# Performance work log

Measured on AMD Instinct MI355X. Metric: run time of the kernel, lower is better.

Reference implementation:

```python
import jax, jax.numpy as jnp
import numpy as np

N, K = 16384, 16          # nodes, neighbors per node
IN, HID, OUT = 256, 512, 512
HEADS, A = 8, 64          # heads * attention_size = 512
EPS = 1e-5


def _layernorm(x, g, b):
    m = x.mean(-1, keepdims=True)
    v = x.var(-1, keepdims=True)
    return (x - m) / jnp.sqrt(v + EPS) * g + b


def setup_inputs() -> dict:
    key = jax.random.key(0)
    ks = jax.random.split(key, 16)
    def lin(k, i, o):
        kw, kb = jax.random.split(k)
        w = jax.random.normal(kw, (i, o), jnp.float32) / np.sqrt(i).astype(np.float32)
        b = jax.random.normal(kb, (o,), jnp.float32) * 0.01
        return w, b
    inp = {}
    inp["data"] = jax.random.normal(ks[0], (N, IN), jnp.float32)
    inp["neighbors"] = jax.random.randint(ks[1], (N, K), 0, N, jnp.int32)
    inp["mlp_w0"], inp["mlp_b0"] = lin(ks[2], IN, HID)
    inp["mlp_w1"], inp["mlp_b1"] = lin(ks[3], HID, HID)
    inp["mlp_w2"], inp["mlp_b2"] = lin(ks[4], HID, HID)
    inp["pd_w"], inp["pd_b"] = lin(ks[5], IN, HID)   # project_down
    inp["pi_w"], inp["pi_b"] = lin(ks[6], IN, OUT)   # project_in
    inp["q_w"], inp["q_b"] = lin(ks[7], HID, HEADS * A)
    inp["k_w"], inp["k_b"] = lin(ks[8], HID, HEADS * A)
    inp["v_w"], inp["v_b"] = lin(ks[9], HID, HEADS * A)
    inp["o_w"], inp["o_b"] = lin(ks[10], HEADS * A, OUT)
    inp["ln1_g"] = jnp.ones((HID,), jnp.float32)
    inp["ln1_b"] = jnp.zeros((HID,), jnp.float32)
    inp["ln2_g"] = jnp.ones((OUT,), jnp.float32)
    inp["ln2_b"] = jnp.zeros((OUT,), jnp.float32)
    return inp


def reference(data, neighbors, mlp_w0, mlp_b0, mlp_w1, mlp_b1, mlp_w2, mlp_b2,
              pd_w, pd_b, pi_w, pi_b, q_w, q_b, k_w, k_b, v_w, v_b, o_w, o_b,
              ln1_g, ln1_b, ln2_g, ln2_b):
    # --- local MLP branch (3-layer MLP, elu between layers) ---
    h = jax.nn.elu(data @ mlp_w0 + mlp_b0)
    h = jax.nn.elu(h @ mlp_w1 + mlp_b1)
    h = h @ mlp_w2 + mlp_b2
    pd = data @ pd_w + pd_b                 # project_down(data), reused twice
    local = h + pd                          # MLP(data) + project_down(data)
    # dropout is identity in eval mode
    local = jax.nn.elu(_layernorm(local + pd, ln1_g, ln1_b))
    # --- neighbour dot multi-head attention ---
    q = (local @ q_w + q_b).reshape(N, HEADS, A)
    kk = (local @ k_w + k_b)
    vv = (local @ v_w + v_b)
    kn = kk[neighbors].reshape(N, K, HEADS, A)   # irregular gather
    vn = vv[neighbors].reshape(N, K, HEADS, A)
    scores = jnp.einsum('nha,nkha->nhk', q, kn) / np.float32(np.sqrt(A))
    w = jax.nn.softmax(scores, axis=-1)
    attn = jnp.einsum('nhk,nkha->nha', w, vn).reshape(N, HEADS * A)
    interaction = attn @ o_w + o_b
    # --- residual + output norm ---
    return _layernorm(interaction + data @ pi_w + pi_b, ln2_g, ln2_b)
```

## Files before the change

### kernel.cpp

```cpp
#include <hip/hip_runtime.h>

typedef _Float16 h16;
typedef _Float16 h16x8 __attribute__((ext_vector_type(8)));
typedef _Float16 h16x4 __attribute__((ext_vector_type(4)));
typedef _Float16 h16x2 __attribute__((ext_vector_type(2)));
typedef float f32x4 __attribute__((ext_vector_type(4)));

#define DEV static __device__ __forceinline__

static constexpr size_t OFF_DATA = 0;
static constexpr size_t OFF_W0T  = 4194304;
static constexpr size_t OFF_W1T  = 4325376;
static constexpr size_t OFF_W2PD = 4587520;
static constexpr size_t OFF_QKVT = 4980736;
static constexpr size_t OFF_OPIT = 5767168;
static constexpr size_t OFF_X1   = 6160384;
static constexpr size_t OFF_X2   = 14548992;
static constexpr size_t OFF_KV   = OFF_X1;
static constexpr size_t OFF_P    = 22937600;

DEV void gload16(const void* g, void* l)
{
    __builtin_amdgcn_global_load_lds(
        (__attribute__((address_space(1))) void*)(void*)g,
        (__attribute__((address_space(3))) void*)l, 16, 0, 0);
}

DEV float eluf(float x) { return x > 0.f ? x : __expf(x) - 1.f; }

__global__ __launch_bounds__(256)
void k_cvt_data(const float* __restrict__ src, h16* __restrict__ dst)
{
    size_t i = ((size_t)blockIdx.x * 256 + threadIdx.x) * 4;
    float4 v = *(const float4*)(src + i);
    h16x4 o;
    o[0] = (h16)v.x; o[1] = (h16)v.y; o[2] = (h16)v.z; o[3] = (h16)v.w;
    *(h16x4*)(dst + i) = o;
}

__global__ void k_prep_w(const float* __restrict__ w0, const float* __restrict__ w1,
                         const float* __restrict__ w2, const float* __restrict__ pdw,
                         const float* __restrict__ qw, const float* __restrict__ kw,
                         const float* __restrict__ vw, const float* __restrict__ ow,
                         const float* __restrict__ piw, h16* __restrict__ ws)
{
    int b = blockIdx.x;
    const float* src; h16* dst; int K, dstStride, dstKOff = 0, tb; float scale = 1.f;
    const int N = 512;
    if (b < 128)       { src = w0;  dst = ws + OFF_W0T;           K = 256; dstStride = 256; tb = 0; }
    else if (b < 384)  { src = w1;  dst = ws + OFF_W1T;           K = 512; dstStride = 512; tb = 128; }
    else if (b < 640)  { src = w2;  dst = ws + OFF_W2PD;          K = 512; dstStride = 768; tb = 384; }
    else if (b < 768)  { src = pdw; dst = ws + OFF_W2PD;          K = 256; dstStride = 768; dstKOff = 512; scale = 2.f; tb = 640; }
    else if (b < 1024) { src = qw;  dst = ws + OFF_QKVT;          K = 512; dstStride = 512; tb = 768; }
    else if (b < 1280) { src = kw;  dst = ws + OFF_QKVT + 262144; K = 512; dstStride = 512; tb = 1024; }
    else if (b < 1536) { src = vw;  dst = ws + OFF_QKVT + 524288; K = 512; dstStride = 512; tb = 1280; }
    else if (b < 1792) { src = ow;  dst = ws + OFF_OPIT;          K = 512; dstStride = 768; tb = 1536; }
    else               { src = piw; dst = ws + OFF_OPIT;          K = 256; dstStride = 768; dstKOff = 512; tb = 1792; }
    int t = b - tb;
    int tilesK = K >> 5;
    int tk = t % tilesK, tn = t / tilesK;
    __shared__ float tile[32][33];
    int tx = threadIdx.x, ty = threadIdx.y;
    #pragma unroll
    for (int r = 0; r < 32; r += 8)
        tile[ty + r][tx] = src[(size_t)(tk * 32 + ty + r) * N + tn * 32 + tx] * scale;
    __syncthreads();
    #pragma unroll
    for (int r = 0; r < 32; r += 8) {
        int n = tn * 32 + ty + r, k = tk * 32 + tx;
        dst[(size_t)n * dstStride + dstKOff + k] = (h16)tile[tx][ty + r];
    }
}

template<int BIASMODE, bool DOELU>
__global__ __launch_bounds__(512, 4)
void k_gemm(const h16* __restrict__ A1, const h16* __restrict__ A2,
            const int K1, const int K2,
            const h16* __restrict__ BT,
            const float* __restrict__ bias1, const float* __restrict__ bias2,
            const float* __restrict__ bias3, const float b2scale,
            h16* __restrict__ out, h16* __restrict__ out2, const int N)
{
    const int Kt = K1 + K2;
    __shared__ __align__(16) h16 sA[128 * 32];
    __shared__ __align__(16) h16 sB[128 * 32];
    const int tid  = threadIdx.x;
    const int lane = tid & 63;
    const int mBase = blockIdx.y * 128, nBase = blockIdx.x * 128;
    const int w  = tid >> 6;
    const int wm = (w >> 2) * 64;
    const int wn = (w & 3) * 32;
    const f32x4 zero = {0.f, 0.f, 0.f, 0.f};
    f32x4 acc[4][2];
    #pragma unroll
    for (int i = 0; i < 4; ++i) {
        #pragma unroll
        for (int j = 0; j < 2; ++j) acc[i][j] = zero;
    }

    const int ldR = tid >> 2;
    const int ldC = (tid & 3) * 8;
    const int lm = lane & 15, lk = (lane >> 4) * 8;

    for (int k0 = 0; k0 < Kt; k0 += 32) {
        const h16* Ab; int Ak, As;
        if (k0 < K1) { Ab = A1; Ak = k0;      As = K1; }
        else         { Ab = A2; Ak = k0 - K1; As = K2; }
        gload16(Ab + (size_t)(mBase + ldR) * As + Ak + ldC, &sA[ldR * 32 + ldC]);
        gload16(BT + (size_t)(nBase + ldR) * Kt + k0 + ldC, &sB[ldR * 32 + ldC]);
        __syncthreads();
        h16x8 af[4], bfr[2];
        #pragma unroll
        for (int i = 0; i < 4; ++i) af[i]  = *(const h16x8*)&sA[(wm + i * 16 + lm) * 32 + lk];
        #pragma unroll
        for (int j = 0; j < 2; ++j) bfr[j] = *(const h16x8*)&sB[(wn + j * 16 + lm) * 32 + lk];
        #pragma unroll
        for (int i = 0; i < 4; ++i) {
            #pragma unroll
            for (int j = 0; j < 2; ++j)
                acc[i][j] = __builtin_amdgcn_mfma_f32_16x16x32_f16(af[i], bfr[j], acc[i][j], 0, 0, 0);
        }
        __syncthreads();
    }

    const int lr4 = (lane >> 4) * 4;
    #pragma unroll
    for (int j = 0; j < 2; ++j) {
        const int col = nBase + wn + j * 16 + lm;
        float bv;
        if (BIASMODE == 0) bv = bias1[col];
        else if (BIASMODE == 1) bv = bias1[col] + b2scale * bias2[col];
        else {
            const int seg = col >> 9;
            const float* bp = seg == 0 ? bias1 : (seg == 1 ? bias2 : bias3);
            bv = bp[col & 511];
        }
        #pragma unroll
        for (int i = 0; i < 4; ++i) {
            const int row0 = mBase + wm + i * 16 + lr4;
            #pragma unroll
            for (int r = 0; r < 4; ++r) {
                float v = acc[i][j][r] + bv;
                if (DOELU) v = eluf(v);
                if (BIASMODE == 2) {
                    if (col < 512) out [(size_t)(row0 + r) * 512  + col]         = (h16)v;
                    else           out2[(size_t)(row0 + r) * 1024 + (col - 512)] = (h16)v;
                } else {
                    out[(size_t)(row0 + r) * N + col] = (h16)v;
                }
            }
        }
    }
}

template<bool DOELU, bool OUTF32>
__global__ __launch_bounds__(256)
void k_ln(const h16* __restrict__ X, const float* __restrict__ g, const float* __restrict__ b,
          h16* __restrict__ outH, float* __restrict__ outF)
{
    const int row  = blockIdx.x * 4 + (threadIdx.x >> 6);
    const int lane = threadIdx.x & 63;
    const h16x8 xv = *(const h16x8*)(X + (size_t)row * 512 + lane * 8);
    float v[8], s = 0.f, ss = 0.f;
    #pragma unroll
    for (int k = 0; k < 8; ++k) { v[k] = (float)xv[k]; s += v[k]; ss += v[k] * v[k]; }
    #pragma unroll
    for (int m = 1; m < 64; m <<= 1) { s += __shfl_xor(s, m, 64); ss += __shfl_xor(ss, m, 64); }
    const float mean = s * (1.f / 512.f);
    const float var  = ss * (1.f / 512.f) - mean * mean;
    const float rstd = rsqrtf(var + 1e-5f);
    #pragma unroll
    for (int k = 0; k < 8; ++k) {
        const int c = lane * 8 + k;
        float y = (v[k] - mean) * rstd * g[c] + b[c];
        if (DOELU) y = eluf(y);
        if (OUTF32) outF[(size_t)row * 512 + c] = y;
        else        outH[(size_t)row * 512 + c] = (h16)y;
    }
}

__global__ __launch_bounds__(256)
void k_attn(const h16* __restrict__ Q, const h16* __restrict__ KV,
            const int* __restrict__ nbr, h16* __restrict__ outA)
{
    const int n = blockIdx.x;
    const int tid = threadIdx.x, lane = tid & 63, wave = tid >> 6;
    __shared__ float sS[8][16];
    __shared__ float sW[8][16];
    __shared__ __align__(16) float sP[2][512];
    const int h = lane >> 3;
    const int cbase = lane * 8;
    const int isV = wave >> 1;
    const int jbase = (wave & 1) * 8;

    h16x8 rows[8];
    #pragma unroll
    for (int r = 0; r < 8; ++r) {
        const int j = nbr[n * 16 + jbase + r];
        rows[r] = *(const h16x8*)&KV[(size_t)j * 1024 + (size_t)isV * 512 + cbase];
    }

    if (!isV) {
        const h16x8 qv = *(const h16x8*)&Q[(size_t)n * 512 + cbase];
        float part[8];
        #pragma unroll
        for (int r = 0; r < 8; ++r) {
            float s = 0.f;
            #pragma unroll
            for (int e = 0; e < 8; ++e) s += (float)qv[e] * (float)rows[r][e];
            part[r] = s;
        }
        #pragma unroll
        for (int m = 1; m < 8; m <<= 1) {
            #pragma unroll
            for (int r = 0; r < 8; ++r) part[r] += __shfl_xor(part[r], m, 64);
        }
        if ((lane & 7) == 0) {
            #pragma unroll
            for (int r = 0; r < 8; ++r) sS[h][jbase + r] = part[r] * 0.125f;
        }
    }
    __syncthreads();

    if (tid < 128) {
        const int hh = tid >> 4, j = tid & 15;
        float s = sS[hh][j];
        float mx = s;
        #pragma unroll
        for (int m = 1; m < 16; m <<= 1) mx = fmaxf(mx, __shfl_xor(mx, m, 64));
        const float e = __expf(s - mx);
        float sum = e;
        #pragma unroll
        for (int m = 1; m < 16; m <<= 1) sum += __shfl_xor(sum, m, 64);
        sW[hh][j] = e / sum;
    }
    __syncthreads();

    if (isV) {
        float acc[8];
        #pragma unroll
        for (int e = 0; e < 8; ++e) acc[e] = 0.f;
        #pragma unroll
        for (int r = 0; r < 8; ++r) {
            const float wj = sW[h][jbase + r];
            #pragma unroll
            for (int e = 0; e < 8; ++e) acc[e] += wj * (float)rows[r][e];
        }
        float* dst = &sP[wave & 1][cbase];
        *(f32x4*)dst       = *(const f32x4*)&acc[0];
        *(f32x4*)(dst + 4) = *(const f32x4*)&acc[4];
    }
    __syncthreads();

    const int c = tid * 2;
    const float v0 = sP[0][c] + sP[1][c];
    const float v1 = sP[0][c + 1] + sP[1][c + 1];
    h16x2 o; o[0] = (h16)v0; o[1] = (h16)v1;
    *(h16x2*)&outA[(size_t)n * 512 + c] = o;
}

extern "C" void kernel_launch(void* const* d_in, const int* in_sizes, int n_in,
                              void* d_out, int out_size, void* d_ws, size_t ws_size,
                              hipStream_t stream)
{
    const float* data = (const float*)d_in[0];
    const int*   nbr  = (const int*)d_in[1];
    const float* w0   = (const float*)d_in[2];
    const float* b0   = (const float*)d_in[3];
    const float* w1   = (const float*)d_in[4];
    const float* b1   = (const float*)d_in[5];
    const float* w2   = (const float*)d_in[6];
    const float* b2   = (const float*)d_in[7];
    const float* pdw  = (const float*)d_in[8];
    const float* pdb  = (const float*)d_in[9];
    const float* piw  = (const float*)d_in[10];
    const float* pib  = (const float*)d_in[11];
    const float* qw   = (const float*)d_in[12];
    const float* qb   = (const float*)d_in[13];
    const float* kw   = (const float*)d_in[14];
    const float* kb   = (const float*)d_in[15];
    const float* vw   = (const float*)d_in[16];
    const float* vb   = (const float*)d_in[17];
    const float* ow   = (const float*)d_in[18];
    const float* ob   = (const float*)d_in[19];
    const float* ln1g = (const float*)d_in[20];
    const float* ln1b = (const float*)d_in[21];
    const float* ln2g = (const float*)d_in[22];
    const float* ln2b = (const float*)d_in[23];
    h16*   ws  = (h16*)d_ws;
    float* out = (float*)d_out;
    h16*   qbuf = (h16*)d_out;

    k_cvt_data<<<4096, 256, 0, stream>>>(data, ws + OFF_DATA);
    k_prep_w<<<1920, dim3(32, 8), 0, stream>>>(w0, w1, w2, pdw, qw, kw, vw, ow, piw, ws);

    dim3 gA(4, 128);
    dim3 gQ(12, 128);
    k_gemm<0, true ><<<gA, 512, 0, stream>>>(ws + OFF_DATA, nullptr, 256, 0, ws + OFF_W0T,
                                             b0, nullptr, nullptr, 0.f,
                                             ws + OFF_X1, nullptr, 512);
    k_gemm<0, true ><<<gA, 512, 0, stream>>>(ws + OFF_X1, nullptr, 512, 0, ws + OFF_W1T,
                                             b1, nullptr, nullptr, 0.f,
                                             ws + OFF_X2, nullptr, 512);
    k_gemm<1, false><<<gA, 512, 0, stream>>>(ws + OFF_X2, ws + OFF_DATA, 512, 256, ws + OFF_W2PD,
                                             b2, pdb, nullptr, 2.f,
                                             ws + OFF_P, nullptr, 512);
    k_ln<true, false><<<4096, 256, 0, stream>>>(ws + OFF_P, ln1g, ln1b, ws + OFF_P, nullptr);
    k_gemm<2, false><<<gQ, 512, 0, stream>>>(ws + OFF_P, nullptr, 512, 0, ws + OFF_QKVT,
                                             qb, kb, vb, 0.f,
                                             qbuf, ws + OFF_KV, 1536);
    k_attn<<<16384, 256, 0, stream>>>(qbuf, ws + OFF_KV, nbr, ws + OFF_P);
    k_gemm<1, false><<<gA, 512, 0, stream>>>(ws + OFF_P, ws + OFF_DATA, 512, 256, ws + OFF_OPIT,
                                             ob, pib, nullptr, 1.f,
                                             ws + OFF_X1, nullptr, 512);
    k_ln<false, true><<<4096, 256, 0, stream>>>(ws + OFF_X1, ln2g, ln2b, nullptr, out);
}
```

Measured before the change: 331.1 us.

## Swizzle GEMM block order across XCDs and process two nodes per attention block

The GEMM grid becomes 1D and is remapped so that eight consecutive block IDs (likely spread round-robin across the eight XCDs) share an N-tile and cover adjacent M rows, aiming to improve L2 reuse of the weight tiles. The attention kernel now handles two nodes per block, issuing both nodes' neighbour gathers up front for more memory-level parallelism and using all 256 threads in the softmax. This raises register pressure in the attention kernel and halves its block count.

```diff
diff --git a/kernel.cpp b/kernel.cpp
--- a/kernel.cpp
+++ b/kernel.cpp
@@ -72,7 +72,7 @@
     }
 }
 
-template<int BIASMODE, bool DOELU>
+template<int BIASMODE, bool DOELU, int NT>
 __global__ __launch_bounds__(512, 4)
 void k_gemm(const h16* __restrict__ A1, const h16* __restrict__ A2,
             const int K1, const int K2,
@@ -86,7 +86,11 @@
     __shared__ __align__(16) h16 sB[128 * 32];
     const int tid  = threadIdx.x;
     const int lane = tid & 63;
-    const int mBase = blockIdx.y * 128, nBase = blockIdx.x * 128;
+    const int bswz = blockIdx.x;
+    const int slot = bswz & 7;
+    const int gg   = bswz >> 3;
+    const int mBase = ((gg / NT) * 8 + slot) * 128;
+    const int nBase = (gg % NT) * 128;
     const int w  = tid >> 6;
     const int wm = (w >> 2) * 64;
     const int wn = (w & 3) * 32;
@@ -183,48 +187,65 @@
 void k_attn(const h16* __restrict__ Q, const h16* __restrict__ KV,
             const int* __restrict__ nbr, h16* __restrict__ outA)
 {
-    const int n = blockIdx.x;
+    const int n0 = blockIdx.x * 2;
     const int tid = threadIdx.x, lane = tid & 63, wave = tid >> 6;
-    __shared__ float sS[8][16];
-    __shared__ float sW[8][16];
-    __shared__ __align__(16) float sP[2][512];
+    __shared__ float sS[2][8][16];
+    __shared__ float sW[2][8][16];
+    __shared__ __align__(16) float sP[2][2][512];
     const int h = lane >> 3;
     const int cbase = lane * 8;
     const int isV = wave >> 1;
     const int jbase = (wave & 1) * 8;
 
-    h16x8 rows[8];
-    #pragma unroll
-    for (int r = 0; r < 8; ++r) {
-        const int j = nbr[n * 16 + jbase + r];
-        rows[r] = *(const h16x8*)&KV[(size_t)j * 1024 + (size_t)isV * 512 + cbase];
-    }
+    int idxA[8], idxB[8];
+    #pragma unroll
+    for (int r = 0; r < 8; ++r) idxA[r] = nbr[n0 * 16 + jbase + r];
+    #pragma unroll
+    for (int r = 0; r < 8; ++r) idxB[r] = nbr[(n0 + 1) * 16 + jbase + r];
+
+    h16x8 rA[8], rB[8];
+    #pragma unroll
+    for (int r = 0; r < 8; ++r)
+        rA[r] = *(const h16x8*)&KV[(size_t)idxA[r] * 1024 + (size_t)isV * 512 + cbase];
+    #pragma unroll
+    for (int r = 0; r < 8; ++r)
+        rB[r] = *(const h16x8*)&KV[(size_t)idxB[r] * 1024 + (size_t)isV * 512 + cbase];
 
     if (!isV) {
-        const h16x8 qv = *(const h16x8*)&Q[(size_t)n * 512 + cbase];
-        float part[8];
+        const h16x8 qA = *(const h16x8*)&Q[(size_t)n0 * 512 + cbase];
+        const h16x8 qB = *(const h16x8*)&Q[(size_t)(n0 + 1) * 512 + cbase];
+        float pA[8], pB[8];
         #pragma unroll
         for (int r = 0; r < 8; ++r) {
-            float s = 0.f;
-            #pragma unroll
-            for (int e = 0; e < 8; ++e) s += (float)qv[e] * (float)rows[r][e];
-            part[r] = s;
+            float sa = 0.f, sb = 0.f;
+            #pragma unroll
+            for (int e = 0; e < 8; ++e) {
+                sa += (float)qA[e] * (float)rA[r][e];
+                sb += (float)qB[e] * (float)rB[r][e];
+            }
+            pA[r] = sa; pB[r] = sb;
         }
         #pragma unroll
         for (int m = 1; m < 8; m <<= 1) {
             #pragma unroll
-            for (int r = 0; r < 8; ++r) part[r] += __shfl_xor(part[r], m, 64);
+            for (int r = 0; r < 8; ++r) {
+                pA[r] += __shfl_xor(pA[r], m, 64);
+                pB[r] += __shfl_xor(pB[r], m, 64);
+            }
         }
         if ((lane & 7) == 0) {
             #pragma unroll
-            for (int r = 0; r < 8; ++r) sS[h][jbase + r] = part[r] * 0.125f;
+            for (int r = 0; r < 8; ++r) {
+                sS[0][h][jbase + r] = pA[r] * 0.125f;
+                sS[1][h][jbase + r] = pB[r] * 0.125f;
+            }
         }
     }
     __syncthreads();
 
-    if (tid < 128) {
-        const int hh = tid >> 4, j = tid & 15;
-        float s = sS[hh][j];
+    {
+        const int nn = tid >> 7, hh = (tid >> 4) & 7, j = tid & 15;
+        float s = sS[nn][hh][j];
         float mx = s;
         #pragma unroll
         for (int m = 1; m < 16; m <<= 1) mx = fmaxf(mx, __shfl_xor(mx, m, 64));
@@ -232,31 +253,41 @@
         float sum = e;
         #pragma unroll
         for (int m = 1; m < 16; m <<= 1) sum += __shfl_xor(sum, m, 64);
-        sW[hh][j] = e / sum;
+        sW[nn][hh][j] = e / sum;
     }
     __syncthreads();
 
     if (isV) {
-        float acc[8];
-        #pragma unroll
-        for (int e = 0; e < 8; ++e) acc[e] = 0.f;
+        float accA[8], accB[8];
+        #pragma unroll
+        for (int e = 0; e < 8; ++e) { accA[e] = 0.f; accB[e] = 0.f; }
         #pragma unroll
         for (int r = 0; r < 8; ++r) {
-            const float wj = sW[h][jbase + r];
-            #pragma unroll
-            for (int e = 0; e < 8; ++e) acc[e] += wj * (float)rows[r][e];
-        }
-        float* dst = &sP[wave & 1][cbase];
-        *(f32x4*)dst       = *(const f32x4*)&acc[0];
-        *(f32x4*)(dst + 4) = *(const f32x4*)&acc[4];
+            const float wa = sW[0][h][jbase + r];
+            const float wb = sW[1][h][jbase + r];
+            #pragma unroll
+            for (int e = 0; e < 8; ++e) {
+                accA[e] += wa * (float)rA[r][e];
+                accB[e] += wb * (float)rB[r][e];
+            }
+        }
+        float* dA = &sP[0][wave & 1][cbase];
+        float* dB = &sP[1][wave & 1][cbase];
+        *(f32x4*)dA       = *(const f32x4*)&accA[0];
+        *(f32x4*)(dA + 4) = *(const f32x4*)&accA[4];
+        *(f32x4*)dB       = *(const f32x4*)&accB[0];
+        *(f32x4*)(dB + 4) = *(const f32x4*)&accB[4];
     }
     __syncthreads();
 
     const int c = tid * 2;
-    const float v0 = sP[0][c] + sP[1][c];
-    const float v1 = sP[0][c + 1] + sP[1][c + 1];
-    h16x2 o; o[0] = (h16)v0; o[1] = (h16)v1;
-    *(h16x2*)&outA[(size_t)n * 512 + c] = o;
+    #pragma unroll
+    for (int nn = 0; nn < 2; ++nn) {
+        const float v0 = sP[nn][0][c] + sP[nn][1][c];
+        const float v1 = sP[nn][0][c + 1] + sP[nn][1][c + 1];
+        h16x2 o; o[0] = (h16)v0; o[1] = (h16)v1;
+        *(h16x2*)&outA[(size_t)(n0 + nn) * 512 + c] = o;
+    }
 }
 
 extern "C" void kernel_launch(void* const* d_in, const int* in_sizes, int n_in,
@@ -294,23 +325,21 @@
     k_cvt_data<<<4096, 256, 0, stream>>>(data, ws + OFF_DATA);
     k_prep_w<<<1920, dim3(32, 8), 0, stream>>>(w0, w1, w2, pdw, qw, kw, vw, ow, piw, ws);
 
-    dim3 gA(4, 128);
-    dim3 gQ(12, 128);
-    k_gemm<0, true ><<<gA, 512, 0, stream>>>(ws + OFF_DATA, nullptr, 256, 0, ws + OFF_W0T,
+    k_gemm<0, true , 4><<<512, 512, 0, stream>>>(ws + OFF_DATA, nullptr, 256, 0, ws + OFF_W0T,
                                              b0, nullptr, nullptr, 0.f,
                                              ws + OFF_X1, nullptr, 512);
-    k_gemm<0, true ><<<gA, 512, 0, stream>>>(ws + OFF_X1, nullptr, 512, 0, ws + OFF_W1T,
+    k_gemm<0, true , 4><<<512, 512, 0, stream>>>(ws + OFF_X1, nullptr, 512, 0, ws + OFF_W1T,
                                              b1, nullptr, nullptr, 0.f,
                                              ws + OFF_X2, nullptr, 512);
-    k_gemm<1, false><<<gA, 512, 0, stream>>>(ws + OFF_X2, ws + OFF_DATA, 512, 256, ws + OFF_W2PD,
+    k_gemm<1, false, 4><<<512, 512, 0, stream>>>(ws + OFF_X2, ws + OFF_DATA, 512, 256, ws + OFF_W2PD,
                                              b2, pdb, nullptr, 2.f,
                                              ws + OFF_P, nullptr, 512);
     k_ln<true, false><<<4096, 256, 0, stream>>>(ws + OFF_P, ln1g, ln1b, ws + OFF_P, nullptr);
-    k_gemm<2, false><<<gQ, 512, 0, stream>>>(ws + OFF_P, nullptr, 512, 0, ws + OFF_QKVT,
+    k_gemm<2, false, 12><<<1536, 512, 0, stream>>>(ws + OFF_P, nullptr, 512, 0, ws + OFF_QKVT,
                                              qb, kb, vb, 0.f,
                                              qbuf, ws + OFF_KV, 1536);
-    k_attn<<<16384, 256, 0, stream>>>(qbuf, ws + OFF_KV, nbr, ws + OFF_P);
-    k_gemm<1, false><<<gA, 512, 0, stream>>>(ws + OFF_P, ws + OFF_DATA, 512, 256, ws + OFF_OPIT,
+    k_attn<<<8192, 256, 0, stream>>>(qbuf, ws + OFF_KV, nbr, ws + OFF_P);
+    k_gemm<1, false, 4><<<512, 512, 0, stream>>>(ws + OFF_P, ws + OFF_DATA, 512, 256, ws + OFF_OPIT,
                                              ob, pib, nullptr, 1.f,
                                              ws + OFF_X1, nullptr, 512);
     k_ln<false, true><<<4096, 256, 0, stream>>>(ws + OFF_X1, ln2g, ln2b, nullptr, out);
```

After: 323.3 us. 1.02x faster.

## Collapse attention into one wave per node and swizzle GEMM block order

Applied to the files above, without the earlier changes.

The attention kernel now runs one 64-lane wave per node. Each lane loads all 16 neighbor K and V rows for its 8 channels and computes the scores, softmax and weighted sum in registers. This removes the shared-memory staging, the three block barriers and the cross-wave reduction, in exchange for more registers per thread. The GEMMs move to a 1D grid with a swizzle that groups 8 M-tiles per N-column block, so that resident blocks share the same weight tiles in cache.

```diff
diff --git a/kernel.cpp b/kernel.cpp
--- a/kernel.cpp
+++ b/kernel.cpp
@@ -72,7 +72,7 @@
     }
 }
 
-template<int BIASMODE, bool DOELU>
+template<int BIASMODE, bool DOELU, int NT>
 __global__ __launch_bounds__(512, 4)
 void k_gemm(const h16* __restrict__ A1, const h16* __restrict__ A2,
             const int K1, const int K2,
@@ -86,7 +86,11 @@
     __shared__ __align__(16) h16 sB[128 * 32];
     const int tid  = threadIdx.x;
     const int lane = tid & 63;
-    const int mBase = blockIdx.y * 128, nBase = blockIdx.x * 128;
+    const int bswz = blockIdx.x;
+    const int slot = bswz & 7;
+    const int gg   = bswz >> 3;
+    const int mBase = ((gg / NT) * 8 + slot) * 128;
+    const int nBase = (gg % NT) * 128;
     const int w  = tid >> 6;
     const int wm = (w >> 2) * 64;
     const int wn = (w & 3) * 32;
@@ -179,84 +183,59 @@
     }
 }
 
-__global__ __launch_bounds__(256)
+__global__ __launch_bounds__(64)
 void k_attn(const h16* __restrict__ Q, const h16* __restrict__ KV,
             const int* __restrict__ nbr, h16* __restrict__ outA)
 {
     const int n = blockIdx.x;
-    const int tid = threadIdx.x, lane = tid & 63, wave = tid >> 6;
-    __shared__ float sS[8][16];
-    __shared__ float sW[8][16];
-    __shared__ __align__(16) float sP[2][512];
-    const int h = lane >> 3;
+    const int lane = threadIdx.x;
     const int cbase = lane * 8;
-    const int isV = wave >> 1;
-    const int jbase = (wave & 1) * 8;
-
-    h16x8 rows[8];
-    #pragma unroll
-    for (int r = 0; r < 8; ++r) {
-        const int j = nbr[n * 16 + jbase + r];
-        rows[r] = *(const h16x8*)&KV[(size_t)j * 1024 + (size_t)isV * 512 + cbase];
-    }
-
-    if (!isV) {
-        const h16x8 qv = *(const h16x8*)&Q[(size_t)n * 512 + cbase];
-        float part[8];
-        #pragma unroll
-        for (int r = 0; r < 8; ++r) {
-            float s = 0.f;
-            #pragma unroll
-            for (int e = 0; e < 8; ++e) s += (float)qv[e] * (float)rows[r][e];
-            part[r] = s;
-        }
-        #pragma unroll
-        for (int m = 1; m < 8; m <<= 1) {
-            #pragma unroll
-            for (int r = 0; r < 8; ++r) part[r] += __shfl_xor(part[r], m, 64);
-        }
-        if ((lane & 7) == 0) {
-            #pragma unroll
-            for (int r = 0; r < 8; ++r) sS[h][jbase + r] = part[r] * 0.125f;
-        }
-    }
-    __syncthreads();
-
-    if (tid < 128) {
-        const int hh = tid >> 4, j = tid & 15;
-        float s = sS[hh][j];
-        float mx = s;
-        #pragma unroll
-        for (int m = 1; m < 16; m <<= 1) mx = fmaxf(mx, __shfl_xor(mx, m, 64));
-        const float e = __expf(s - mx);
-        float sum = e;
-        #pragma unroll
-        for (int m = 1; m < 16; m <<= 1) sum += __shfl_xor(sum, m, 64);
-        sW[hh][j] = e / sum;
-    }
-    __syncthreads();
-
-    if (isV) {
-        float acc[8];
-        #pragma unroll
-        for (int e = 0; e < 8; ++e) acc[e] = 0.f;
-        #pragma unroll
-        for (int r = 0; r < 8; ++r) {
-            const float wj = sW[h][jbase + r];
-            #pragma unroll
-            for (int e = 0; e < 8; ++e) acc[e] += wj * (float)rows[r][e];
-        }
-        float* dst = &sP[wave & 1][cbase];
-        *(f32x4*)dst       = *(const f32x4*)&acc[0];
-        *(f32x4*)(dst + 4) = *(const f32x4*)&acc[4];
-    }
-    __syncthreads();
-
-    const int c = tid * 2;
-    const float v0 = sP[0][c] + sP[1][c];
-    const float v1 = sP[0][c + 1] + sP[1][c + 1];
-    h16x2 o; o[0] = (h16)v0; o[1] = (h16)v1;
-    *(h16x2*)&outA[(size_t)n * 512 + c] = o;
+
+    const h16x8 qv = *(const h16x8*)&Q[(size_t)n * 512 + cbase];
+
+    h16x8 kr[16], vr[16];
+    #pragma unroll
+    for (int j = 0; j < 16; ++j) {
+        const int idx = nbr[n * 16 + j];
+        const h16* base = &KV[(size_t)idx * 1024 + cbase];
+        kr[j] = *(const h16x8*)base;
+        vr[j] = *(const h16x8*)(base + 512);
+    }
+
+    float s[16];
+    #pragma unroll
+    for (int j = 0; j < 16; ++j) {
+        float d = 0.f;
+        #pragma unroll
+        for (int e = 0; e < 8; ++e) d += (float)qv[e] * (float)kr[j][e];
+        s[j] = d;
+    }
+    #pragma unroll
+    for (int m = 1; m < 8; m <<= 1) {
+        #pragma unroll
+        for (int j = 0; j < 16; ++j) s[j] += __shfl_xor(s[j], m, 64);
+    }
+    float mx = -1e30f;
+    #pragma unroll
+    for (int j = 0; j < 16; ++j) { s[j] *= 0.125f; mx = fmaxf(mx, s[j]); }
+    float sum = 0.f;
+    #pragma unroll
+    for (int j = 0; j < 16; ++j) { s[j] = __expf(s[j] - mx); sum += s[j]; }
+    const float rinv = 1.f / sum;
+
+    float acc[8];
+    #pragma unroll
+    for (int e = 0; e < 8; ++e) acc[e] = 0.f;
+    #pragma unroll
+    for (int j = 0; j < 16; ++j) {
+        const float w = s[j] * rinv;
+        #pragma unroll
+        for (int e = 0; e < 8; ++e) acc[e] += w * (float)vr[j][e];
+    }
+    h16x8 o;
+    #pragma unroll
+    for (int e = 0; e < 8; ++e) o[e] = (h16)acc[e];
+    *(h16x8*)&outA[(size_t)n * 512 + cbase] = o;
 }
 
 extern "C" void kernel_launch(void* const* d_in, const int* in_sizes, int n_in,
@@ -294,23 +273,21 @@
     k_cvt_data<<<4096, 256, 0, stream>>>(data, ws + OFF_DATA);
     k_prep_w<<<1920, dim3(32, 8), 0, stream>>>(w0, w1, w2, pdw, qw, kw, vw, ow, piw, ws);
 
-    dim3 gA(4, 128);
-    dim3 gQ(12, 128);
-    k_gemm<0, true ><<<gA, 512, 0, stream>>>(ws + OFF_DATA, nullptr, 256, 0, ws + OFF_W0T,
+    k_gemm<0, true , 4><<<512, 512, 0, stream>>>(ws + OFF_DATA, nullptr, 256, 0, ws + OFF_W0T,
                                              b0, nullptr, nullptr, 0.f,
                                              ws + OFF_X1, nullptr, 512);
-    k_gemm<0, true ><<<gA, 512, 0, stream>>>(ws + OFF_X1, nullptr, 512, 0, ws + OFF_W1T,
+    k_gemm<0, true , 4><<<512, 512, 0, stream>>>(ws + OFF_X1, nullptr, 512, 0, ws + OFF_W1T,
                                              b1, nullptr, nullptr, 0.f,
                                              ws + OFF_X2, nullptr, 512);
-    k_gemm<1, false><<<gA, 512, 0, stream>>>(ws + OFF_X2, ws + OFF_DATA, 512, 256, ws + OFF_W2PD,
+    k_gemm<1, false, 4><<<512, 512, 0, stream>>>(ws + OFF_X2, ws + OFF_DATA, 512, 256, ws + OFF_W2PD,
                                              b2, pdb, nullptr, 2.f,
                                              ws + OFF_P, nullptr, 512);
     k_ln<true, false><<<4096, 256, 0, stream>>>(ws + OFF_P, ln1g, ln1b, ws + OFF_P, nullptr);
-    k_gemm<2, false><<<gQ, 512, 0, stream>>>(ws + OFF_P, nullptr, 512, 0, ws + OFF_QKVT,
+    k_gemm<2, false, 12><<<1536, 512, 0, stream>>>(ws + OFF_P, nullptr, 512, 0, ws + OFF_QKVT,
                                              qb, kb, vb, 0.f,
                                              qbuf, ws + OFF_KV, 1536);
-    k_attn<<<16384, 256, 0, stream>>>(qbuf, ws + OFF_KV, nbr, ws + OFF_P);
-    k_gemm<1, false><<<gA, 512, 0, stream>>>(ws + OFF_P, ws + OFF_DATA, 512, 256, ws + OFF_OPIT,
+    k_attn<<<16384, 64, 0, stream>>>(qbuf, ws + OFF_KV, nbr, ws + OFF_P);
+    k_gemm<1, false, 4><<<512, 512, 0, stream>>>(ws + OFF_P, ws + OFF_DATA, 512, 256, ws + OFF_OPIT,
                                              ob, pib, nullptr, 1.f,
                                              ws + OFF_X1, nullptr, 512);
     k_ln<false, true><<<4096, 256, 0, stream>>>(ws + OFF_X1, ln2g, ln2b, nullptr, out);
```

Result: faster. 321.3 us (-3.0%).
